# Kernel optimization log

Measured on AMD Instinct MI355X. Metric: run time of the kernel, lower is better.

The kernel has to match this reference:

```python
import jax, jax.numpy as jnp
import numpy as np

B, S, DM, H = 2, 2048, 1024, 16        # dim_model = d_model//2 = 1024
WINDOW, DILATION, N_GLOBAL = 513, 2, 32
HD = DM // H
NEG = -1e9


def build_mask(n, window_size, dilation, global_idx):
    # dilated local window: |i-j| <= (window//2)*dilation and (i-j) % dilation == 0
    i = jnp.arange(n)[:, None]
    j = jnp.arange(n)[None, :]
    d = j - i
    half = window_size // 2
    local = (jnp.abs(d) <= half * dilation) & (jnp.mod(d, dilation) == 0)
    g = jnp.zeros((n,), bool).at[global_idx].set(True)
    # symmetric global token mask: global rows and columns fully attend
    return local | g[:, None] | g[None, :]


def setup_inputs() -> dict:
    key = jax.random.key(0)
    ks = jax.random.split(key, 9)
    std = 0.02
    inp = {
        "q": jax.random.normal(ks[0], (B, S, DM), jnp.float32),
        "k": jax.random.normal(ks[1], (B, S, DM), jnp.float32),
        "v": jax.random.normal(ks[2], (B, S, DM), jnp.float32),
        "Wq": jax.random.normal(ks[3], (DM, DM), jnp.float32) * std,
        "Wk": jax.random.normal(ks[4], (DM, DM), jnp.float32) * std,
        "Wv": jax.random.normal(ks[5], (DM, DM), jnp.float32) * std,
        "Wo": jax.random.normal(ks[6], (DM, DM), jnp.float32) * std,
        "bq": jnp.zeros((DM,), jnp.float32),
        "bk": jnp.zeros((DM,), jnp.float32),
        "bv": jnp.zeros((DM,), jnp.float32),
        "bo": jnp.zeros((DM,), jnp.float32),
        "global_idx": jax.random.randint(ks[7], (N_GLOBAL,), 0, S, jnp.int64)
        if jax.config.jax_enable_x64 else jax.random.randint(ks[7], (N_GLOBAL,), 0, S, jnp.int32),
    }
    return inp


def reference(q, k, v, Wq, Wk, Wv, Wo, bq, bk, bv, bo, global_idx):
    def split(x):  # [B,S,DM] -> [B,H,S,HD]
        return x.reshape(B, S, H, HD).transpose(0, 2, 1, 3)

    qh = split(q @ Wq.T + bq)
    kh = split(k @ Wk.T + bk)
    vh = split(v @ Wv.T + bv)

    scores = jnp.einsum("bhqd,bhkd->bhqk", qh, kh) / jnp.sqrt(jnp.asarray(HD, qh.dtype))
    mask = build_mask(S, WINDOW, DILATION, global_idx)  # [S,S] bool
    scores = jnp.where(mask[None, None], scores, NEG)
    attn = jax.nn.softmax(scores, axis=-1)
    out = jnp.einsum("bhqk,bhkd->bhqd", attn, vh)
    out = out.transpose(0, 2, 1, 3).reshape(B, S, DM)
    return out @ Wo.T + bo
```

## Files before the change

kernel.cpp:

```cpp
#include <hip/hip_runtime.h>
#include <hip/hip_bf16.h>
#include <math.h>

#define BB 2
#define SS 2048
#define DMM 1024
#define HH 16
#define HDD 64
#define NGLOB 32
#define MM 4096
#define SCALE2 0.18033688f

typedef __attribute__((ext_vector_type(8))) short short8;
typedef __attribute__((ext_vector_type(4))) float float4v;

__device__ __forceinline__ short f2bf(float f) {
    union { float f; unsigned u; } x; x.f = f;
    unsigned r = (x.u + 0x7fffu + ((x.u >> 16) & 1u)) >> 16;
    return (short)r;
}

#define ASYNC16(gp, lp) __builtin_amdgcn_global_load_lds( \
    (__attribute__((address_space(1))) void*)(gp), \
    (__attribute__((address_space(3))) void*)(lp), 16, 0, 0)

#define VSL(dim, key) ((dim) * 40 + (((((key) >> 3) ^ (((dim) >> 3) & 3)) << 3) | ((key) & 7)))

__global__ void setup_globals(const int* __restrict__ gidx, int* __restrict__ g,
                              int* __restrict__ glist, int* __restrict__ gcount) {
    int t = threadIdx.x;
    for (int i = t; i < SS; i += 256) g[i] = 0;
    if (t == 0) *gcount = 0;
    __syncthreads();
    if (t < NGLOB) {
        int j = gidx[t];
        if (j >= 0 && j < SS) g[j] = 1;
    }
    __syncthreads();
    for (int j = t; j < SS; j += 256) {
        if (g[j]) {
            int p = atomicAdd(gcount, 1);
            glist[p] = j;
        }
    }
}

__global__ __launch_bounds__(256)
void convert_all(const float* __restrict__ q, const float* __restrict__ k,
                 const float* __restrict__ v,
                 const float* __restrict__ w0, const float* __restrict__ w1,
                 const float* __restrict__ w2, const float* __restrict__ w3,
                 short* __restrict__ abf, short* __restrict__ wbf) {
    int z = blockIdx.y;
    const float* src;
    short* dst;
    size_t n;
    if (z < 3) {
        src = (z == 0) ? q : (z == 1) ? k : v;
        dst = abf + (size_t)z * ((size_t)MM * DMM);
        n = (size_t)MM * DMM;
    } else {
        int y = z - 3;
        src = (y == 0) ? w0 : (y == 1) ? w1 : (y == 2) ? w2 : w3;
        dst = wbf + (size_t)y * ((size_t)DMM * DMM);
        n = (size_t)DMM * DMM;
    }
    size_t i = ((size_t)blockIdx.x * 256 + threadIdx.x) * 8;
    if (i >= n) return;
    float4 a = *(const float4*)(src + i);
    float4 b = *(const float4*)(src + i + 4);
    short8 s;
    s[0]=f2bf(a.x); s[1]=f2bf(a.y); s[2]=f2bf(a.z); s[3]=f2bf(a.w);
    s[4]=f2bf(b.x); s[5]=f2bf(b.y); s[6]=f2bf(b.z); s[7]=f2bf(b.w);
    *(short8*)(dst + i) = s;
}

template<int OBF, int HEADSPLIT>
__global__ __launch_bounds__(256)
void gemm128(const short* __restrict__ Abase, const short* __restrict__ Wbase,
             const float* __restrict__ b0, const float* __restrict__ b1,
             const float* __restrict__ b2,
             void* __restrict__ O0p, void* __restrict__ O1p, void* __restrict__ O2p) {
    __shared__ short As[128 * 32];
    __shared__ short Ws[128 * 32];

    int t = threadIdx.x;
    int z = blockIdx.y;
    const short* A    = Abase + (size_t)z * ((size_t)MM * DMM);
    const short* W    = Wbase + (size_t)z * ((size_t)DMM * DMM);
    const float* bias = (z == 0) ? b0 : (z == 1) ? b1 : b2;
    void* outp        = (z == 0) ? O0p : (z == 1) ? O1p : O2p;

    int bid = blockIdx.x;
    int xcd = bid & 7, loc = bid >> 3;
    int nblk = loc & 7, mloc = loc >> 3;
    int m0 = (xcd * 4 + mloc) * 128;
    int n0 = nblk * 128;

    int lane = t & 63, w = t >> 6;
    int quad = lane >> 4, col = lane & 15;
    int wr = (w & 1) * 64;
    int wc = (w >> 1) * 64;

    float4v acc[4][4];
    #pragma unroll
    for (int i = 0; i < 4; i++)
        #pragma unroll
        for (int j = 0; j < 4; j++) acc[i][j] = (float4v){0, 0, 0, 0};

    int rowA = t >> 2,  kcA = (t & 3) * 8;

    for (int it = 0; it < 32; it++) {
        int k0 = it * 32;
        ASYNC16(A + (size_t)(m0 + rowA) * DMM + k0 + kcA,      &As[t * 8]);
        ASYNC16(A + (size_t)(m0 + 64 + rowA) * DMM + k0 + kcA, &As[2048 + t * 8]);
        ASYNC16(W + (size_t)(n0 + rowA) * DMM + k0 + kcA,      &Ws[t * 8]);
        ASYNC16(W + (size_t)(n0 + 64 + rowA) * DMM + k0 + kcA, &Ws[2048 + t * 8]);
        __syncthreads();

        short8 aF[4], bF[4];
        #pragma unroll
        for (int i = 0; i < 4; i++)
            aF[i] = *(short8*)&As[(wr + 16 * i + col) * 32 + quad * 8];
        #pragma unroll
        for (int j = 0; j < 4; j++)
            bF[j] = *(short8*)&Ws[(wc + 16 * j + col) * 32 + quad * 8];

        #pragma unroll
        for (int i = 0; i < 4; i++)
            #pragma unroll
            for (int j = 0; j < 4; j++)
                acc[i][j] = __builtin_amdgcn_mfma_f32_16x16x32_bf16(aF[i], bF[j], acc[i][j], 0, 0, 0);
        __syncthreads();
    }

    #pragma unroll
    for (int i = 0; i < 4; i++) {
        #pragma unroll
        for (int j = 0; j < 4; j++) {
            int n = n0 + wc + 16 * j + col;
            float bn = bias[n];
            #pragma unroll
            for (int r = 0; r < 4; r++) {
                int m = m0 + wr + 16 * i + quad * 4 + r;
                float val = acc[i][j][r] + bn;
                size_t idx;
                if (HEADSPLIT) {
                    int b = m >> 11;
                    int s = m & 2047;
                    int h = n >> 6;
                    int hd = n & 63;
                    idx = (((size_t)b * HH + h) * SS + s) * HDD + hd;
                } else {
                    idx = (size_t)m * DMM + n;
                }
                if (OBF) ((short*)outp)[idx] = f2bf(val);
                else     ((float*)outp)[idx] = val;
            }
        }
    }
}

__global__ __launch_bounds__(256)
void band_attn(const short* __restrict__ qh, const short* __restrict__ kh,
               const short* __restrict__ vh, const int* __restrict__ glist,
               const int* __restrict__ gcount, short* __restrict__ ao) {
    __shared__ short Qs[64 * 72];
    __shared__ short Ks[32 * 72];
    __shared__ short Vt[64 * 40];
    __shared__ short Ps[4 * 16 * 40];
    __shared__ int   gjs[32];

    int t = threadIdx.x;
    int bid = blockIdx.x;
    int xcd = bid & 7, idx = bid >> 3;
    int gl  = idx >> 4;
    int qt  = idx & 15;
    int gid = xcd * 8 + gl;
    int z   = gid >> 4;
    int h   = gid & 15;
    int b = z >> 1, p = z & 1;
    int qq0 = qt * 64;
    int nG = *gcount;

    const short* Qb = qh + ((size_t)(b * HH + h) * SS) * HDD;
    const short* Kb = kh + ((size_t)(b * HH + h) * SS) * HDD;
    const short* Vb = vh + ((size_t)(b * HH + h) * SS) * HDD;

    int row8 = t >> 3;
    int dim8 = (t & 7) * 8;

    #pragma unroll
    for (int rr = 0; rr < 2; rr++) {
        int row = rr * 32 + row8;
        int i = 2 * (qq0 + row) + p;
        short8 qv = *(const short8*)(Qb + (size_t)i * HDD + dim8);
        *(short8*)&Qs[row * 72 + dim8] = qv;
    }
    if (t < 32) gjs[t] = (t < nG) ? glist[t] : -1000000;
    __syncthreads();

    int lane = t & 63, w = t >> 6;
    int quad = lane >> 4, col = lane & 15;

    short8 qf0 = *(short8*)&Qs[(16 * w + col) * 72 + quad * 8];
    short8 qf1 = *(short8*)&Qs[(16 * w + col) * 72 + 32 + quad * 8];

    float4v O0 = {0,0,0,0}, O1 = {0,0,0,0}, O2 = {0,0,0,0}, O3 = {0,0,0,0};
    float lst[4] = {0.f, 0.f, 0.f, 0.f};

    for (int c = 0; c < 19; c++) {
        __syncthreads();
        int ch0 = qq0 - 256 + c * 32;
        int srow;
        if (c < 18) srow = 2 * (ch0 + row8) + p;
        else        srow = (row8 < nG) ? gjs[row8] : 0;
        srow = srow < 0 ? 0 : (srow > SS - 1 ? SS - 1 : srow);
        short8 kv = *(const short8*)(Kb + (size_t)srow * HDD + dim8);
        short8 vv = *(const short8*)(Vb + (size_t)srow * HDD + dim8);
        *(short8*)&Ks[row8 * 72 + dim8] = kv;
        #pragma unroll
        for (int j = 0; j < 8; j++) {
            int d = dim8 + j;
            Vt[VSL(d, row8)] = vv[j];
        }
        __syncthreads();

        short8 kA0 = *(short8*)&Ks[col * 72 + quad * 8];
        short8 kA1 = *(short8*)&Ks[col * 72 + 32 + quad * 8];
        short8 kB0 = *(short8*)&Ks[(16 + col) * 72 + quad * 8];
        short8 kB1 = *(short8*)&Ks[(16 + col) * 72 + 32 + quad * 8];
        float4v sA = {0,0,0,0}, sB = {0,0,0,0};
        sA = __builtin_amdgcn_mfma_f32_16x16x32_bf16(qf0, kA0, sA, 0, 0, 0);
        sA = __builtin_amdgcn_mfma_f32_16x16x32_bf16(qf1, kA1, sA, 0, 0, 0);
        sB = __builtin_amdgcn_mfma_f32_16x16x32_bf16(qf0, kB0, sB, 0, 0, 0);
        sB = __builtin_amdgcn_mfma_f32_16x16x32_bf16(qf1, kB1, sB, 0, 0, 0);

        if (c < 18) {
            int nlo = -ch0;
            int nhi = 1023 - ch0;
            #pragma unroll
            for (int r = 0; r < 4; r++) {
                int qq = qq0 + 16 * w + quad * 4 + r;
                int u  = qq - ch0;
                int lo = max(u - 256, nlo);
                int hi = min(u + 256, nhi);
                bool vA = (col >= lo) && (col <= hi);
                bool vB = (col + 16 >= lo) && (col + 16 <= hi);
                float pa = vA ? exp2f(sA[r] * SCALE2) : 0.f;
                float pb = vB ? exp2f(sB[r] * SCALE2) : 0.f;
                lst[r] += pa + pb;
                Ps[(w * 16 + quad * 4 + r) * 40 + col]      = f2bf(pa);
                Ps[(w * 16 + quad * 4 + r) * 40 + col + 16] = f2bf(pb);
            }
        } else {
            #pragma unroll
            for (int r = 0; r < 4; r++) {
                int qq = qq0 + 16 * w + quad * 4 + r;
                int i = 2 * qq + p;
                int jA = gjs[col], jB = gjs[col + 16];
                int dA = jA - i, dB = jB - i;
                int aA = dA < 0 ? -dA : dA;
                int aB = dB < 0 ? -dB : dB;
                bool vA = (jA >= 0) && !((aA <= 512) && ((dA & 1) == 0));
                bool vB = (jB >= 0) && !((aB <= 512) && ((dB & 1) == 0));
                float pa = vA ? exp2f(sA[r] * SCALE2) : 0.f;
                float pb = vB ? exp2f(sB[r] * SCALE2) : 0.f;
                lst[r] += pa + pb;
                Ps[(w * 16 + quad * 4 + r) * 40 + col]      = f2bf(pa);
                Ps[(w * 16 + quad * 4 + r) * 40 + col + 16] = f2bf(pb);
            }
        }
        asm volatile("s_waitcnt lgkmcnt(0)" ::: "memory");

        short8 pf  = *(short8*)&Ps[(w * 16 + col) * 40 + quad * 8];
        short8 vf0 = *(short8*)&Vt[(col) * 40 + ((quad ^ ((col >> 3) & 3)) << 3)];
        short8 vf1 = *(short8*)&Vt[(16 + col) * 40 + ((quad ^ (((16 + col) >> 3) & 3)) << 3)];
        short8 vf2 = *(short8*)&Vt[(32 + col) * 40 + ((quad ^ (((32 + col) >> 3) & 3)) << 3)];
        short8 vf3 = *(short8*)&Vt[(48 + col) * 40 + ((quad ^ (((48 + col) >> 3) & 3)) << 3)];
        O0 = __builtin_amdgcn_mfma_f32_16x16x32_bf16(pf, vf0, O0, 0, 0, 0);
        O1 = __builtin_amdgcn_mfma_f32_16x16x32_bf16(pf, vf1, O1, 0, 0, 0);
        O2 = __builtin_amdgcn_mfma_f32_16x16x32_bf16(pf, vf2, O2, 0, 0, 0);
        O3 = __builtin_amdgcn_mfma_f32_16x16x32_bf16(pf, vf3, O3, 0, 0, 0);
    }

    #pragma unroll
    for (int r = 0; r < 4; r++) {
        float l = lst[r];
        #pragma unroll
        for (int mk = 1; mk < 16; mk <<= 1) l += __shfl_xor(l, mk);
        float inv = 1.0f / l;
        int q = 16 * w + quad * 4 + r;
        int i = 2 * (qq0 + q) + p;
        short* dst = ao + ((size_t)b * SS + i) * DMM + h * HDD;
        dst[col]      = f2bf(O0[r] * inv);
        dst[col + 16] = f2bf(O1[r] * inv);
        dst[col + 32] = f2bf(O2[r] * inv);
        dst[col + 48] = f2bf(O3[r] * inv);
    }
}

__global__ __launch_bounds__(256)
void global_part(const short* __restrict__ qh, const short* __restrict__ kh,
                 const short* __restrict__ vh, const int* __restrict__ glist,
                 const int* __restrict__ gcount,
                 float* __restrict__ pl, float* __restrict__ pO) {
    __shared__ short Qs[32 * 72];
    __shared__ short Ks[2][32 * 72];
    __shared__ short Vt[2][64 * 40];
    __shared__ short Ps[4 * 16 * 40];

    int t = threadIdx.x;
    int s = blockIdx.x, h = blockIdx.y, b = blockIdx.z;
    int nG = *gcount;

    const short* Qb = qh + ((size_t)(b * HH + h) * SS) * HDD;
    const short* Kb = kh + ((size_t)(b * HH + h) * SS) * HDD;
    const short* Vb = vh + ((size_t)(b * HH + h) * SS) * HDD;

    int row8 = t >> 3, dim8 = (t & 7) * 8;
    {
        int cq = row8 < nG ? row8 : 0;
        int src = glist[cq];
        short8 qv = *(const short8*)(Qb + (size_t)src * HDD + dim8);
        *(short8*)&Qs[row8 * 72 + dim8] = qv;
    }
    __syncthreads();

    int lane = t & 63, w = t >> 6;
    int quad = lane >> 4, col = lane & 15;
    int g = w >> 1, qt = w & 1;

    short8 qf0 = *(short8*)&Qs[(qt * 16 + col) * 72 + quad * 8];
    short8 qf1 = *(short8*)&Qs[(qt * 16 + col) * 72 + 32 + quad * 8];

    float4v O0 = {0,0,0,0}, O1 = {0,0,0,0}, O2 = {0,0,0,0}, O3 = {0,0,0,0};
    float lst[4] = {0.f, 0.f, 0.f, 0.f};

    int js0 = s * 256;
    for (int it = 0; it < 4; it++) {
        __syncthreads();
        int r64 = t >> 2, dimb = (t & 3) * 16;
        int j = js0 + it * 64 + r64;
        const short* kp = Kb + (size_t)j * HDD + dimb;
        const short* vp = Vb + (size_t)j * HDD + dimb;
        short8 k0 = *(const short8*)kp, k1 = *(const short8*)(kp + 8);
        short8 v0 = *(const short8*)vp, v1 = *(const short8*)(vp + 8);
        int half = r64 >> 5, r32 = r64 & 31;
        *(short8*)&Ks[half][r32 * 72 + dimb]     = k0;
        *(short8*)&Ks[half][r32 * 72 + dimb + 8] = k1;
        #pragma unroll
        for (int u = 0; u < 8; u++) {
            int d = dimb + u;
            Vt[half][VSL(d, r32)] = v0[u];
        }
        #pragma unroll
        for (int u = 0; u < 8; u++) {
            int d = dimb + 8 + u;
            Vt[half][VSL(d, r32)] = v1[u];
        }
        __syncthreads();

        short8 kA0 = *(short8*)&Ks[g][col * 72 + quad * 8];
        short8 kA1 = *(short8*)&Ks[g][col * 72 + 32 + quad * 8];
        short8 kB0 = *(short8*)&Ks[g][(16 + col) * 72 + quad * 8];
        short8 kB1 = *(short8*)&Ks[g][(16 + col) * 72 + 32 + quad * 8];
        float4v sA = {0,0,0,0}, sB = {0,0,0,0};
        sA = __builtin_amdgcn_mfma_f32_16x16x32_bf16(qf0, kA0, sA, 0, 0, 0);
        sA = __builtin_amdgcn_mfma_f32_16x16x32_bf16(qf1, kA1, sA, 0, 0, 0);
        sB = __builtin_amdgcn_mfma_f32_16x16x32_bf16(qf0, kB0, sB, 0, 0, 0);
        sB = __builtin_amdgcn_mfma_f32_16x16x32_bf16(qf1, kB1, sB, 0, 0, 0);

        #pragma unroll
        for (int r = 0; r < 4; r++) {
            float pa = exp2f(sA[r] * SCALE2);
            float pb = exp2f(sB[r] * SCALE2);
            lst[r] += pa + pb;
            Ps[(w * 16 + quad * 4 + r) * 40 + col]      = f2bf(pa);
            Ps[(w * 16 + quad * 4 + r) * 40 + col + 16] = f2bf(pb);
        }
        asm volatile("s_waitcnt lgkmcnt(0)" ::: "memory");

        short8 pf  = *(short8*)&Ps[(w * 16 + col) * 40 + quad * 8];
        short8 vf0 = *(short8*)&Vt[g][(col) * 40 + ((quad ^ ((col >> 3) & 3)) << 3)];
        short8 vf1 = *(short8*)&Vt[g][(16 + col) * 40 + ((quad ^ (((16 + col) >> 3) & 3)) << 3)];
        short8 vf2 = *(short8*)&Vt[g][(32 + col) * 40 + ((quad ^ (((32 + col) >> 3) & 3)) << 3)];
        short8 vf3 = *(short8*)&Vt[g][(48 + col) * 40 + ((quad ^ (((48 + col) >> 3) & 3)) << 3)];
        O0 = __builtin_amdgcn_mfma_f32_16x16x32_bf16(pf, vf0, O0, 0, 0, 0);
        O1 = __builtin_amdgcn_mfma_f32_16x16x32_bf16(pf, vf1, O1, 0, 0, 0);
        O2 = __builtin_amdgcn_mfma_f32_16x16x32_bf16(pf, vf2, O2, 0, 0, 0);
        O3 = __builtin_amdgcn_mfma_f32_16x16x32_bf16(pf, vf3, O3, 0, 0, 0);
    }

    int sp = s * 2 + g;
    size_t base = ((size_t)(b * HH + h) * 16 + sp) * 32;
    #pragma unroll
    for (int r = 0; r < 4; r++) {
        float l = lst[r];
        #pragma unroll
        for (int mk = 1; mk < 16; mk <<= 1) l += __shfl_xor(l, mk);
        int q = qt * 16 + quad * 4 + r;
        if (col == 0) pl[base + q] = l;
        float* Od = pO + (base + q) * 64;
        Od[col]      = O0[r];
        Od[col + 16] = O1[r];
        Od[col + 32] = O2[r];
        Od[col + 48] = O3[r];
    }
}

__global__ __launch_bounds__(256)
void global_merge(const float* __restrict__ pl, const float* __restrict__ pO,
                  const int* __restrict__ glist, const int* __restrict__ gcount,
                  short* __restrict__ ao) {
    int h = blockIdx.x, b = blockIdx.y;
    int t = threadIdx.x;
    int d = t & 63, qg = t >> 6;
    int nG = *gcount;
    size_t bh = ((size_t)(b * HH + h) * 16) * 32;

    for (int q = qg; q < nG; q += 4) {
        float L = 0.f, acc = 0.f;
        #pragma unroll
        for (int sp = 0; sp < 16; sp++) {
            L   += pl[bh + sp * 32 + q];
            acc += pO[(bh + sp * 32 + q) * 64 + d];
        }
        int i = glist[q];
        ao[((size_t)b * SS + i) * DMM + h * HDD + d] = f2bf(acc / L);
    }
}

extern "C" void kernel_launch(void* const* d_in, const int* in_sizes, int n_in,
                              void* d_out, int out_size, void* d_ws, size_t ws_size,
                              hipStream_t stream) {
    const float* q  = (const float*)d_in[0];
    const float* k  = (const float*)d_in[1];
    const float* v  = (const float*)d_in[2];
    const float* Wq = (const float*)d_in[3];
    const float* Wk = (const float*)d_in[4];
    const float* Wv = (const float*)d_in[5];
    const float* Wo = (const float*)d_in[6];
    const float* bq = (const float*)d_in[7];
    const float* bk = (const float*)d_in[8];
    const float* bv = (const float*)d_in[9];
    const float* bo = (const float*)d_in[10];
    const int* gidx = (const int*)d_in[11];
    float* out = (float*)d_out;

    const size_t NE = (size_t)BB * SS * DMM;
    const size_t WE = (size_t)DMM * DMM;
    int*   g      = (int*)d_ws;
    int*   glist  = g + SS;
    int*   gcount = glist + SS;
    short* qh     = (short*)((char*)d_ws + 32768);
    short* kh     = qh + NE;
    short* vh     = kh + NE;
    short* ao     = vh + NE;
    short* wbf    = ao + NE;
    short* wo     = wbf + 3 * WE;
    short* abf    = wbf + 4 * WE;
    float* pl     = (float*)abf;
    float* pO     = pl + 16384;

    setup_globals<<<1, 256, 0, stream>>>(gidx, g, glist, gcount);

    dim3 gc(2048, 7);
    convert_all<<<gc, 256, 0, stream>>>(q, k, v, Wq, Wk, Wv, Wo, abf, wbf);

    dim3 gq(256, 3);
    gemm128<1, 1><<<gq, 256, 0, stream>>>(abf, wbf, bq, bk, bv, qh, kh, vh);

    band_attn<<<1024, 256, 0, stream>>>(qh, kh, vh, glist, gcount, ao);

    dim3 gp(8, HH, BB);
    global_part<<<gp, 256, 0, stream>>>(qh, kh, vh, glist, gcount, pl, pO);

    dim3 gm(HH, BB);
    global_merge<<<gm, 256, 0, stream>>>(pl, pO, glist, gcount, ao);

    dim3 go(256, 1);
    gemm128<0, 0><<<go, 256, 0, stream>>>(ao, wo, bo, bo, bo, out, out, out);
}
```

Before: 240.7 us.

## Triple-buffer GEMM LDS tiles with async prefetch two stages ahead

The projection GEMM now keeps three LDS buffers per operand and issues the global-to-LDS async loads for iteration it+2 while computing on the current buffer. It waits with a partial vmcnt instead of a full barrier-drain, and drops one of the two barriers per iteration. The goal is to hide global load latency behind MFMA work. In exchange LDS use triples, which may lower occupancy, and correctness relies on the vmcnt count matching the number of loads in flight.

```diff
diff --git a/kernel.cpp b/kernel.cpp
--- a/kernel.cpp
+++ b/kernel.cpp
@@ -81,8 +81,8 @@
              const float* __restrict__ b0, const float* __restrict__ b1,
              const float* __restrict__ b2,
              void* __restrict__ O0p, void* __restrict__ O1p, void* __restrict__ O2p) {
-    __shared__ short As[128 * 32];
-    __shared__ short Ws[128 * 32];
+    __shared__ short As[3][128 * 32];
+    __shared__ short Ws[3][128 * 32];
 
     int t = threadIdx.x;
     int z = blockIdx.y;
@@ -109,30 +109,45 @@
         for (int j = 0; j < 4; j++) acc[i][j] = (float4v){0, 0, 0, 0};
 
     int rowA = t >> 2,  kcA = (t & 3) * 8;
-
+    const short* Ap = A + (size_t)(m0 + rowA) * DMM + kcA;
+    const short* Wp = W + (size_t)(n0 + rowA) * DMM + kcA;
+
+    #define STAGE(bf, tt) do { int kk = (tt) * 32; \
+        ASYNC16(Ap + kk,                      &As[bf][t * 8]); \
+        ASYNC16(Ap + 64 * (size_t)DMM + kk,   &As[bf][2048 + t * 8]); \
+        ASYNC16(Wp + kk,                      &Ws[bf][t * 8]); \
+        ASYNC16(Wp + 64 * (size_t)DMM + kk,   &Ws[bf][2048 + t * 8]); \
+    } while (0)
+
+    STAGE(0, 0);
+    STAGE(1, 1);
+
+    int cur = 0;
     for (int it = 0; it < 32; it++) {
-        int k0 = it * 32;
-        ASYNC16(A + (size_t)(m0 + rowA) * DMM + k0 + kcA,      &As[t * 8]);
-        ASYNC16(A + (size_t)(m0 + 64 + rowA) * DMM + k0 + kcA, &As[2048 + t * 8]);
-        ASYNC16(W + (size_t)(n0 + rowA) * DMM + k0 + kcA,      &Ws[t * 8]);
-        ASYNC16(W + (size_t)(n0 + 64 + rowA) * DMM + k0 + kcA, &Ws[2048 + t * 8]);
-        __syncthreads();
+        if (it < 31) asm volatile("s_waitcnt vmcnt(4)" ::: "memory");
+        else         asm volatile("s_waitcnt vmcnt(0)" ::: "memory");
+        __builtin_amdgcn_s_barrier();
+
+        int sb = cur - 1; if (sb < 0) sb = 2;
+        if (it + 2 < 32) STAGE(sb, it + 2);
 
         short8 aF[4], bF[4];
         #pragma unroll
         for (int i = 0; i < 4; i++)
-            aF[i] = *(short8*)&As[(wr + 16 * i + col) * 32 + quad * 8];
+            aF[i] = *(short8*)&As[cur][(wr + 16 * i + col) * 32 + quad * 8];
         #pragma unroll
         for (int j = 0; j < 4; j++)
-            bF[j] = *(short8*)&Ws[(wc + 16 * j + col) * 32 + quad * 8];
+            bF[j] = *(short8*)&Ws[cur][(wc + 16 * j + col) * 32 + quad * 8];
 
         #pragma unroll
         for (int i = 0; i < 4; i++)
             #pragma unroll
             for (int j = 0; j < 4; j++)
                 acc[i][j] = __builtin_amdgcn_mfma_f32_16x16x32_bf16(aF[i], bF[j], acc[i][j], 0, 0, 0);
-        __syncthreads();
-    }
+
+        cur++; if (cur == 3) cur = 0;
+    }
+    #undef STAGE
 
     #pragma unroll
     for (int i = 0; i < 4; i++) {
```

New measurement: 236.3 us. Within noise of the previous version (-1.8%).
